# Performance work log

Measured on AMD Instinct MI355X. Metric: run time of the kernel, lower is better.

Reference implementation:

```python
import jax, jax.numpy as jnp
import numpy as np

B, S, D_MODEL, D_FF, NUM_EXPERTS, TOP_K = 2, 2048, 1024, 4096, 8, 2


def setup_inputs() -> dict:
    key = jax.random.key(0)
    ks = jax.random.split(key, 5)
    scale = 0.02
    return {
        "x": jax.random.normal(ks[0], (B, S, D_MODEL), jnp.float32),
        # gate: Linear(d_model, num_experts, bias=False); stored as [d_model, E]
        "Wg": jax.random.normal(ks[1], (D_MODEL, NUM_EXPERTS), jnp.float32) * scale,
        # stacked expert FFN params
        "W1": jax.random.normal(ks[2], (NUM_EXPERTS, D_MODEL, D_FF), jnp.float32) * scale,
        "b1": jnp.zeros((NUM_EXPERTS, D_FF), jnp.float32),
        "W2": jax.random.normal(ks[3], (NUM_EXPERTS, D_FF, D_MODEL), jnp.float32) * scale,
        "b2": jnp.zeros((NUM_EXPERTS, D_MODEL), jnp.float32),
    }


def _moe_forward(x, Wg, W1, b1, W2, b2):
    b, s, d = x.shape
    xt = x.reshape(-1, d)                       # [T, d]
    T = xt.shape[0]
    # --- TopKRouter ---
    probs = jax.nn.softmax(xt @ Wg, axis=-1)    # [T, E]
    w, idx = jax.lax.top_k(probs, TOP_K)        # [T, K]
    w = w / jnp.sum(w, axis=-1, keepdims=True)  # renormalize top-k weights
    # scatter routing weights into dense per-expert combine weights [T, E]
    gate = jnp.zeros((T, Wg.shape[1]), xt.dtype)
    gate = gate.at[jnp.arange(T)[:, None], idx].add(w)
    # --- per-expert FFN, weighted combine (scan over experts, E is small) ---
    def body(out, params):
        W1e, b1e, W2e, b2e, ge = params
        h = jax.nn.relu(xt @ W1e + b1e)         # [T, d_ff]
        out = out + (h @ W2e + b2e) * ge[:, None]
        return out, None
    out0 = jnp.zeros_like(xt)
    out, _ = jax.lax.scan(body, out0, (W1, b1, W2, b2, gate.T))
    return out.reshape(b, s, d)


def reference(x, Wg, W1, b1, W2, b2):
    # eval mode: dropout = identity, load-balance loss = None -> return output only
    return _moe_forward(x, Wg, W1, b1, W2, b2)
```

## Files before the change

### kernel.cpp

```cpp
#include <hip/hip_runtime.h>
#include <hip/hip_bf16.h>
#include <cstdint>
#include <cstddef>

#define T_TOK 4096
#define DM 1024
#define DFF 4096
#define NE 8
#define BT 128
#define BK 64
#define PADCAP (T_TOK * 2 + NE * BT)
#define MTILES (PADCAP / BT)

typedef __attribute__((ext_vector_type(8))) short short8;
typedef __attribute__((ext_vector_type(4))) float f32x4;

__device__ __forceinline__ unsigned short f2bf(float f) {
  unsigned int u = __float_as_uint(f);
  return (unsigned short)((u + 0x7fff + ((u >> 16) & 1)) >> 16);
}
__device__ __forceinline__ float bf2f(unsigned short u) {
  return __uint_as_float((unsigned int)u << 16);
}

__device__ __forceinline__ void load_lds16(const void* g, void* l) {
  __builtin_amdgcn_global_load_lds(
      (const __attribute__((address_space(1))) int*)g,
      (__attribute__((address_space(3))) int*)l, 16, 0, 0);
}

#define WAIT_VM8() __builtin_amdgcn_s_waitcnt(0x0F78)
#define WAIT_VM0() __builtin_amdgcn_s_waitcnt(0x0F70)
#define BARRIER()                          \
  do {                                     \
    __asm__ volatile("" ::: "memory");     \
    __builtin_amdgcn_s_barrier();          \
    __asm__ volatile("" ::: "memory");     \
  } while (0)

__global__ __launch_bounds__(256) void gate_kernel(
    const float* __restrict__ x, const float* __restrict__ Wg,
    int* __restrict__ counts, int* __restrict__ topk_idx,
    float* __restrict__ topk_w, unsigned short* __restrict__ xb) {
  int gid = blockIdx.x * blockDim.x + threadIdx.x;
  int t = gid >> 6;
  int lane = gid & 63;
  if (t >= T_TOK) return;
  const float* xr = x + (size_t)t * DM;
  unsigned short* xbr = xb + (size_t)t * DM;
  float acc[NE];
#pragma unroll
  for (int e = 0; e < NE; ++e) acc[e] = 0.f;
#pragma unroll
  for (int j = 0; j < DM / 64; ++j) {
    int d = lane + j * 64;
    float xv = xr[d];
    xbr[d] = f2bf(xv);
    const float4* wr = (const float4*)(Wg + (size_t)d * NE);
    float4 w0 = wr[0], w1 = wr[1];
    acc[0] += xv * w0.x; acc[1] += xv * w0.y;
    acc[2] += xv * w0.z; acc[3] += xv * w0.w;
    acc[4] += xv * w1.x; acc[5] += xv * w1.y;
    acc[6] += xv * w1.z; acc[7] += xv * w1.w;
  }
#pragma unroll
  for (int off = 32; off >= 1; off >>= 1) {
#pragma unroll
    for (int e = 0; e < NE; ++e) acc[e] += __shfl_xor(acc[e], off, 64);
  }
  if (lane == 0) {
    int i0 = 0;
#pragma unroll
    for (int e = 1; e < NE; ++e)
      if (acc[e] > acc[i0]) i0 = e;
    int i1 = (i0 == 0) ? 1 : 0;
#pragma unroll
    for (int e = 0; e < NE; ++e)
      if (e != i0 && acc[e] > acc[i1]) i1 = e;
    float e1 = __expf(acc[i1] - acc[i0]);
    float inv = 1.f / (1.f + e1);
    topk_idx[t * 2] = i0;
    topk_idx[t * 2 + 1] = i1;
    topk_w[t * 2] = inv;
    topk_w[t * 2 + 1] = e1 * inv;
    atomicAdd(&counts[i0], 1);
    atomicAdd(&counts[i1], 1);
  }
}

__global__ void init_kernel(int* counts, int* cursors, int* bucket_tok) {
  int i = blockIdx.x * blockDim.x + threadIdx.x;
  if (i < NE) { counts[i] = 0; cursors[i] = 0; }
  if (i < PADCAP) bucket_tok[i] = -1;
}

__global__ void offsets_kernel(const int* __restrict__ counts,
                               int* __restrict__ offsets) {
  if (threadIdx.x == 0) {
    int o = 0;
    offsets[0] = 0;
    for (int e = 0; e < NE; ++e) {
      o += (counts[e] + BT - 1) & ~(BT - 1);
      offsets[e + 1] = o;
    }
  }
}

__global__ void scatter_kernel(const int* __restrict__ topk_idx,
                               const int* __restrict__ offsets,
                               int* __restrict__ cursors,
                               int* __restrict__ bucket_tok,
                               int* __restrict__ slot_of) {
  int t = blockIdx.x * blockDim.x + threadIdx.x;
  if (t >= T_TOK) return;
#pragma unroll
  for (int k = 0; k < 2; ++k) {
    int e = topk_idx[t * 2 + k];
    int pos = atomicAdd(&cursors[e], 1);
    int slot = offsets[e] + pos;
    bucket_tok[slot] = t;
    slot_of[t * 2 + k] = slot;
  }
}

__global__ __launch_bounds__(256) void transpose_cvt_kernel(
    const float* __restrict__ W, unsigned short* __restrict__ Wt,
    int K, int N) {
  __shared__ float Ls[64][68];
  int e = blockIdx.z;
  const float* We = W + (size_t)e * K * N;
  unsigned short* Wte = Wt + (size_t)e * K * N;
  int k0 = blockIdx.x * 64, n0 = blockIdx.y * 64;
  int tid = threadIdx.x;
  int kr = tid >> 4, nf = (tid & 15) * 4;
#pragma unroll
  for (int p = 0; p < 4; ++p) {
    int k = kr + p * 16;
    float4 v = *(const float4*)(We + (size_t)(k0 + k) * N + n0 + nf);
    Ls[k][nf] = v.x; Ls[k][nf + 1] = v.y;
    Ls[k][nf + 2] = v.z; Ls[k][nf + 3] = v.w;
  }
  __syncthreads();
#pragma unroll
  for (int i = 0; i < 2; ++i) {
    int id = tid + i * 256;
    int n = id >> 3, kc = id & 7;
    short8 hv;
#pragma unroll
    for (int j = 0; j < 8; ++j) hv[j] = (short)f2bf(Ls[kc * 8 + j][n]);
    *(short8*)(Wte + (size_t)(n0 + n) * K + k0 + kc * 8) = hv;
  }
}


__global__ __launch_bounds__(256) void gemm1_kernel(
    const unsigned short* __restrict__ xb, const unsigned short* __restrict__ Wt1,
    const float* __restrict__ b1, const int* __restrict__ offsets,
    const int* __restrict__ bucket_tok, unsigned short* __restrict__ h) {
  int r0 = blockIdx.x * BT;
  if (r0 >= offsets[NE]) return;
  int e = 0;
  while (offsets[e + 1] <= r0) ++e;
  int n0 = blockIdx.y * 128;

  __shared__ __align__(16) short As[2 * 128 * 64];
  __shared__ __align__(16) short Bs[2 * 128 * 64];
  __shared__ int toks[BT];

  int tid = threadIdx.x;
  if (tid < BT) toks[tid] = bucket_tok[r0 + tid];
  __syncthreads();

  int lane = tid & 63, w = tid >> 6;
  int rsub = lane >> 3, kc = lane & 7;
  int jsw = (kc ^ rsub) * 8;
  const unsigned short* ga[4];
  const unsigned short* gb[4];
#pragma unroll
  for (int i = 0; i < 4; ++i) {
    int m = w * 32 + i * 8 + rsub;
    int tk = toks[m]; if (tk < 0) tk = 0;
    ga[i] = xb + (size_t)tk * DM + jsw;
    gb[i] = Wt1 + ((size_t)e * DFF + n0 + m) * DM + jsw;
  }
  int ldsW = w * 2048 + lane * 8;

  int wm = w & 1, wn = w >> 1;
  int g = lane >> 4, l15 = lane & 15;
  int x7 = l15 & 7;
  int csel0 = (g ^ x7) * 8;
  int csel1 = ((4 + g) ^ x7) * 8;

  f32x4 acc[4][4];
#pragma unroll
  for (int i = 0; i < 4; ++i)
#pragma unroll
    for (int jj = 0; jj < 4; ++jj) acc[i][jj] = (f32x4){0.f, 0.f, 0.f, 0.f};

#pragma unroll
  for (int i = 0; i < 4; ++i) {
    load_lds16(ga[i], &As[ldsW + i * 512]);
    load_lds16(gb[i], &Bs[ldsW + i * 512]);
  }

  int buf = 0;
  const int NIT = DM / BK;
  for (int it = 0; it < NIT; ++it) {
    if (it + 1 < NIT) {
      int ko = (it + 1) * BK;
      int dst = (buf ^ 1) * 8192 + ldsW;
#pragma unroll
      for (int i = 0; i < 4; ++i) {
        load_lds16(ga[i] + ko, &As[dst + i * 512]);
        load_lds16(gb[i] + ko, &Bs[dst + i * 512]);
      }
      WAIT_VM8();
    } else {
      WAIT_VM0();
    }
    BARRIER();
    int bb = buf * 8192;
#pragma unroll
    for (int ks = 0; ks < 2; ++ks) {
      int cs = ks ? csel1 : csel0;
      short8 af[4], bfr[4];
#pragma unroll
      for (int mi = 0; mi < 4; ++mi)
        af[mi] = *(const short8*)&As[bb + (wm * 64 + mi * 16 + l15) * 64 + cs];
#pragma unroll
      for (int nj = 0; nj < 4; ++nj)
        bfr[nj] = *(const short8*)&Bs[bb + (wn * 64 + nj * 16 + l15) * 64 + cs];
#pragma unroll
      for (int mi = 0; mi < 4; ++mi)
#pragma unroll
        for (int nj = 0; nj < 4; ++nj)
          acc[mi][nj] = __builtin_amdgcn_mfma_f32_16x16x32_bf16(
              af[mi], bfr[nj], acc[mi][nj], 0, 0, 0);
    }
    BARRIER();
    buf ^= 1;
  }

  const float* b1e = b1 + (size_t)e * DFF;
#pragma unroll
  for (int nj = 0; nj < 4; ++nj) {
    int n = n0 + wn * 64 + nj * 16 + l15;
    float bv = b1e[n];
#pragma unroll
    for (int mi = 0; mi < 4; ++mi) {
      int mb = r0 + wm * 64 + mi * 16 + g * 4;
#pragma unroll
      for (int r = 0; r < 4; ++r) {
        float v = acc[mi][nj][r] + bv;
        h[(size_t)(mb + r) * DFF + n] = f2bf(fmaxf(v, 0.f));
      }
    }
  }
}

__global__ __launch_bounds__(256) void gemm2_kernel(
    const unsigned short* __restrict__ h, const unsigned short* __restrict__ Wt2,
    const float* __restrict__ b2, const int* __restrict__ offsets,
    unsigned short* __restrict__ S) {
  int r0 = blockIdx.y * BT;
  if (r0 >= offsets[NE]) return;
  int e = 0;
  while (offsets[e + 1] <= r0) ++e;
  int n0 = (blockIdx.x & 7) * 128;
  int z = blockIdx.x >> 3;
  int kbeg = z * (DFF / 2);

  __shared__ __align__(16) short As[2 * 128 * 64];
  __shared__ __align__(16) short Bs[2 * 128 * 64];

  int tid = threadIdx.x;
  int lane = tid & 63, w = tid >> 6;
  int rsub = lane >> 3, kc = lane & 7;
  int jsw = (kc ^ rsub) * 8;
  const unsigned short* ga[4];
  const unsigned short* gb[4];
#pragma unroll
  for (int i = 0; i < 4; ++i) {
    int m = w * 32 + i * 8 + rsub;
    ga[i] = h + ((size_t)(r0 + m)) * DFF + kbeg + jsw;
    gb[i] = Wt2 + ((size_t)e * DM + n0 + m) * DFF + kbeg + jsw;
  }
  int ldsW = w * 2048 + lane * 8;

  int wm = w & 1, wn = w >> 1;
  int g = lane >> 4, l15 = lane & 15;
  int x7 = l15 & 7;
  int csel0 = (g ^ x7) * 8;
  int csel1 = ((4 + g) ^ x7) * 8;

  f32x4 acc[4][4];
#pragma unroll
  for (int i = 0; i < 4; ++i)
#pragma unroll
    for (int jj = 0; jj < 4; ++jj) acc[i][jj] = (f32x4){0.f, 0.f, 0.f, 0.f};

#pragma unroll
  for (int i = 0; i < 4; ++i) {
    load_lds16(ga[i], &As[ldsW + i * 512]);
    load_lds16(gb[i], &Bs[ldsW + i * 512]);
  }

  int buf = 0;
  const int NIT = (DFF / 2) / BK;
  for (int it = 0; it < NIT; ++it) {
    if (it + 1 < NIT) {
      int ko = (it + 1) * BK;
      int dst = (buf ^ 1) * 8192 + ldsW;
#pragma unroll
      for (int i = 0; i < 4; ++i) {
        load_lds16(ga[i] + ko, &As[dst + i * 512]);
        load_lds16(gb[i] + ko, &Bs[dst + i * 512]);
      }
      WAIT_VM8();
    } else {
      WAIT_VM0();
    }
    BARRIER();
    int bb = buf * 8192;
#pragma unroll
    for (int ks = 0; ks < 2; ++ks) {
      int cs = ks ? csel1 : csel0;
      short8 af[4], bfr[4];
#pragma unroll
      for (int mi = 0; mi < 4; ++mi)
        af[mi] = *(const short8*)&As[bb + (wm * 64 + mi * 16 + l15) * 64 + cs];
#pragma unroll
      for (int nj = 0; nj < 4; ++nj)
        bfr[nj] = *(const short8*)&Bs[bb + (wn * 64 + nj * 16 + l15) * 64 + cs];
#pragma unroll
      for (int mi = 0; mi < 4; ++mi)
#pragma unroll
        for (int nj = 0; nj < 4; ++nj)
          acc[mi][nj] = __builtin_amdgcn_mfma_f32_16x16x32_bf16(
              af[mi], bfr[nj], acc[mi][nj], 0, 0, 0);
    }
    BARRIER();
    buf ^= 1;
  }

  const float* b2e = b2 + (size_t)e * DM;
  float bscale = (z == 0) ? 1.f : 0.f;
  unsigned short* Sz = S + (size_t)z * PADCAP * DM;
#pragma unroll
  for (int nj = 0; nj < 4; ++nj) {
    int n = n0 + wn * 64 + nj * 16 + l15;
    float bv = b2e[n] * bscale;
#pragma unroll
    for (int mi = 0; mi < 4; ++mi) {
      int mb = r0 + wm * 64 + mi * 16 + g * 4;
#pragma unroll
      for (int r = 0; r < 4; ++r)
        Sz[(size_t)(mb + r) * DM + n] = f2bf(acc[mi][nj][r] + bv);
    }
  }
}

__global__ __launch_bounds__(256) void combine_kernel(
    const unsigned short* __restrict__ S, const int* __restrict__ slot_of,
    const float* __restrict__ topk_w, float* __restrict__ out) {
  int gid = blockIdx.x * 256 + threadIdx.x;
  int t = gid >> 7;
  int c = (gid & 127) * 8;
  int s0 = slot_of[t * 2], s1 = slot_of[t * 2 + 1];
  float w0 = topk_w[t * 2], w1 = topk_w[t * 2 + 1];
  const short8 a0 = *(const short8*)(S + (size_t)s0 * DM + c);
  const short8 a1 = *(const short8*)(S + ((size_t)PADCAP + s0) * DM + c);
  const short8 b0 = *(const short8*)(S + (size_t)s1 * DM + c);
  const short8 b1 = *(const short8*)(S + ((size_t)PADCAP + s1) * DM + c);
  float o[8];
#pragma unroll
  for (int j = 0; j < 8; ++j) {
    float va = bf2f((unsigned short)a0[j]) + bf2f((unsigned short)a1[j]);
    float vb = bf2f((unsigned short)b0[j]) + bf2f((unsigned short)b1[j]);
    o[j] = w0 * va + w1 * vb;
  }
  float* op = out + (size_t)t * DM + c;
  *(float4*)op = (float4){o[0], o[1], o[2], o[3]};
  *(float4*)(op + 4) = (float4){o[4], o[5], o[6], o[7]};
}

extern "C" void kernel_launch(void* const* d_in, const int* in_sizes, int n_in,
                              void* d_out, int out_size, void* d_ws,
                              size_t ws_size, hipStream_t stream) {
  const float* x = (const float*)d_in[0];
  const float* Wg = (const float*)d_in[1];
  const float* W1 = (const float*)d_in[2];
  const float* b1 = (const float*)d_in[3];
  const float* W2 = (const float*)d_in[4];
  const float* b2 = (const float*)d_in[5];
  float* out = (float*)d_out;

  int* ws_i = (int*)d_ws;
  int* counts = ws_i;
  int* offsets = ws_i + 8;
  int* cursors = ws_i + 20;
  int* bucket_tok = ws_i + 32;
  int* topk_idx = ws_i + 32 + PADCAP;
  float* topk_w = (float*)(ws_i + 32 + PADCAP + 2 * T_TOK);
  int* slot_of = ws_i + 32 + PADCAP + 4 * T_TOK;

  const size_t XB_OFF = 1u << 20;
  const size_t WT_OFF = XB_OFF + (size_t)T_TOK * DM * 2;
  const size_t H_OFF = WT_OFF + (size_t)NE * DM * DFF * 2;
  const size_t S_OFF = H_OFF + (size_t)PADCAP * DFF * 2;
  unsigned short* xb = (unsigned short*)((char*)d_ws + XB_OFF);
  unsigned short* Wt = (unsigned short*)((char*)d_ws + WT_OFF);
  unsigned short* h = (unsigned short*)((char*)d_ws + H_OFF);
  unsigned short* S = (unsigned short*)((char*)d_ws + S_OFF);

  init_kernel<<<(PADCAP + 255) / 256, 256, 0, stream>>>(counts, cursors,
                                                        bucket_tok);
  gate_kernel<<<T_TOK / 4, 256, 0, stream>>>(x, Wg, counts, topk_idx, topk_w,
                                             xb);
  offsets_kernel<<<1, 64, 0, stream>>>(counts, offsets);
  scatter_kernel<<<T_TOK / 256, 256, 0, stream>>>(topk_idx, offsets, cursors,
                                                  bucket_tok, slot_of);
  transpose_cvt_kernel<<<dim3(DM / 64, DFF / 64, NE), 256, 0, stream>>>(
      W1, Wt, DM, DFF);
  gemm1_kernel<<<dim3(MTILES, DFF / 128), 256, 0, stream>>>(
      xb, Wt, b1, offsets, bucket_tok, h);
  transpose_cvt_kernel<<<dim3(DFF / 64, DM / 64, NE), 256, 0, stream>>>(
      W2, Wt, DFF, DM);
  gemm2_kernel<<<dim3(16, MTILES), 256, 0, stream>>>(h, Wt, b2, offsets, S);
  combine_kernel<<<(T_TOK * DM / 8) / 256, 256, 0, stream>>>(S, slot_of,
                                                             topk_w, out);
}
```

Baseline: 710.9 us.

## Halve GEMM K-tile to raise occupancy and stage epilogue stores through LDS

Reduces the K tile of both expert GEMMs from 64 to 32, halving LDS use per block and requesting four blocks per CU via launch bounds, with the swizzle and wait counts adjusted to match. The epilogues now write bf16 results into swizzled LDS tiles and then emit 16-byte coalesced global stores instead of scattered 2-byte stores. The transpose kernel's LDS padding also changes. Smaller K tiles double the barrier count per unit of work, and the higher occupancy target may force register spills.

```diff
diff --git a/kernel.cpp b/kernel.cpp
--- a/kernel.cpp
+++ b/kernel.cpp
@@ -8,7 +8,7 @@
 #define DFF 4096
 #define NE 8
 #define BT 128
-#define BK 64
+#define BK 32
 #define PADCAP (T_TOK * 2 + NE * BT)
 #define MTILES (PADCAP / BT)
 
@@ -29,7 +29,7 @@
       (__attribute__((address_space(3))) int*)l, 16, 0, 0);
 }
 
-#define WAIT_VM8() __builtin_amdgcn_s_waitcnt(0x0F78)
+#define WAIT_VM4() __builtin_amdgcn_s_waitcnt(0x0F74)
 #define WAIT_VM0() __builtin_amdgcn_s_waitcnt(0x0F70)
 #define BARRIER()                          \
   do {                                     \
@@ -126,7 +126,7 @@
 __global__ __launch_bounds__(256) void transpose_cvt_kernel(
     const float* __restrict__ W, unsigned short* __restrict__ Wt,
     int K, int N) {
-  __shared__ float Ls[64][68];
+  __shared__ float Ls[64][67];
   int e = blockIdx.z;
   const float* We = W + (size_t)e * K * N;
   unsigned short* Wte = Wt + (size_t)e * K * N;
@@ -153,7 +153,7 @@
 }
 
 
-__global__ __launch_bounds__(256) void gemm1_kernel(
+__global__ __launch_bounds__(256, 4) void gemm1_kernel(
     const unsigned short* __restrict__ xb, const unsigned short* __restrict__ Wt1,
     const float* __restrict__ b1, const int* __restrict__ offsets,
     const int* __restrict__ bucket_tok, unsigned short* __restrict__ h) {
@@ -163,8 +163,8 @@
   while (offsets[e + 1] <= r0) ++e;
   int n0 = blockIdx.y * 128;
 
-  __shared__ __align__(16) short As[2 * 128 * 64];
-  __shared__ __align__(16) short Bs[2 * 128 * 64];
+  __shared__ __align__(16) short As[2 * 128 * 32];
+  __shared__ __align__(16) short Bs[2 * 128 * 32];
   __shared__ int toks[BT];
 
   int tid = threadIdx.x;
@@ -172,24 +172,22 @@
   __syncthreads();
 
   int lane = tid & 63, w = tid >> 6;
-  int rsub = lane >> 3, kc = lane & 7;
-  int jsw = (kc ^ rsub) * 8;
-  const unsigned short* ga[4];
-  const unsigned short* gb[4];
-#pragma unroll
-  for (int i = 0; i < 4; ++i) {
-    int m = w * 32 + i * 8 + rsub;
+  int rsub = lane >> 2, kc = lane & 3;
+  int jsw = (kc ^ (rsub & 3)) * 8;
+  const unsigned short* ga[2];
+  const unsigned short* gb[2];
+#pragma unroll
+  for (int i = 0; i < 2; ++i) {
+    int m = w * 32 + i * 16 + rsub;
     int tk = toks[m]; if (tk < 0) tk = 0;
     ga[i] = xb + (size_t)tk * DM + jsw;
     gb[i] = Wt1 + ((size_t)e * DFF + n0 + m) * DM + jsw;
   }
-  int ldsW = w * 2048 + lane * 8;
+  int ldsW = w * 1024 + lane * 8;
 
   int wm = w & 1, wn = w >> 1;
   int g = lane >> 4, l15 = lane & 15;
-  int x7 = l15 & 7;
-  int csel0 = (g ^ x7) * 8;
-  int csel1 = ((4 + g) ^ x7) * 8;
+  int cs = (g ^ (l15 & 3)) * 8;
 
   f32x4 acc[4][4];
 #pragma unroll
@@ -198,7 +196,7 @@
     for (int jj = 0; jj < 4; ++jj) acc[i][jj] = (f32x4){0.f, 0.f, 0.f, 0.f};
 
 #pragma unroll
-  for (int i = 0; i < 4; ++i) {
+  for (int i = 0; i < 2; ++i) {
     load_lds16(ga[i], &As[ldsW + i * 512]);
     load_lds16(gb[i], &Bs[ldsW + i * 512]);
   }
@@ -208,57 +206,63 @@
   for (int it = 0; it < NIT; ++it) {
     if (it + 1 < NIT) {
       int ko = (it + 1) * BK;
-      int dst = (buf ^ 1) * 8192 + ldsW;
-#pragma unroll
-      for (int i = 0; i < 4; ++i) {
+      int dst = (buf ^ 1) * 4096 + ldsW;
+#pragma unroll
+      for (int i = 0; i < 2; ++i) {
         load_lds16(ga[i] + ko, &As[dst + i * 512]);
         load_lds16(gb[i] + ko, &Bs[dst + i * 512]);
       }
-      WAIT_VM8();
+      WAIT_VM4();
     } else {
       WAIT_VM0();
     }
     BARRIER();
-    int bb = buf * 8192;
-#pragma unroll
-    for (int ks = 0; ks < 2; ++ks) {
-      int cs = ks ? csel1 : csel0;
-      short8 af[4], bfr[4];
-#pragma unroll
-      for (int mi = 0; mi < 4; ++mi)
-        af[mi] = *(const short8*)&As[bb + (wm * 64 + mi * 16 + l15) * 64 + cs];
+    int bb = buf * 4096;
+    short8 af[4], bfr[4];
+#pragma unroll
+    for (int mi = 0; mi < 4; ++mi)
+      af[mi] = *(const short8*)&As[bb + (wm * 64 + mi * 16 + l15) * 32 + cs];
+#pragma unroll
+    for (int nj = 0; nj < 4; ++nj)
+      bfr[nj] = *(const short8*)&Bs[bb + (wn * 64 + nj * 16 + l15) * 32 + cs];
+#pragma unroll
+    for (int mi = 0; mi < 4; ++mi)
 #pragma unroll
       for (int nj = 0; nj < 4; ++nj)
-        bfr[nj] = *(const short8*)&Bs[bb + (wn * 64 + nj * 16 + l15) * 64 + cs];
-#pragma unroll
-      for (int mi = 0; mi < 4; ++mi)
-#pragma unroll
-        for (int nj = 0; nj < 4; ++nj)
-          acc[mi][nj] = __builtin_amdgcn_mfma_f32_16x16x32_bf16(
-              af[mi], bfr[nj], acc[mi][nj], 0, 0, 0);
-    }
+        acc[mi][nj] = __builtin_amdgcn_mfma_f32_16x16x32_bf16(
+            af[mi], bfr[nj], acc[mi][nj], 0, 0, 0);
     BARRIER();
     buf ^= 1;
   }
 
+  unsigned short* wt =
+      (unsigned short*)(w < 2 ? (void*)As : (void*)Bs) + (w & 1) * 4096;
   const float* b1e = b1 + (size_t)e * DFF;
 #pragma unroll
   for (int nj = 0; nj < 4; ++nj) {
-    int n = n0 + wn * 64 + nj * 16 + l15;
-    float bv = b1e[n];
+    int nl = nj * 16 + l15;
+    float bv = b1e[n0 + wn * 64 + nl];
+    int tchunk = nl >> 3, nin = nl & 7;
 #pragma unroll
     for (int mi = 0; mi < 4; ++mi) {
-      int mb = r0 + wm * 64 + mi * 16 + g * 4;
 #pragma unroll
       for (int r = 0; r < 4; ++r) {
+        int ml = mi * 16 + g * 4 + r;
         float v = acc[mi][nj][r] + bv;
-        h[(size_t)(mb + r) * DFF + n] = f2bf(fmaxf(v, 0.f));
+        wt[ml * 64 + (tchunk ^ (ml & 7)) * 8 + nin] = f2bf(fmaxf(v, 0.f));
       }
     }
   }
-}
-
-__global__ __launch_bounds__(256) void gemm2_kernel(
+  int q = lane >> 3, c = lane & 7;
+#pragma unroll
+  for (int i = 0; i < 8; ++i) {
+    int ml = i * 8 + q;
+    short8 v = *(const short8*)&wt[ml * 64 + (c ^ (ml & 7)) * 8];
+    *(short8*)(h + (size_t)(r0 + wm * 64 + ml) * DFF + n0 + wn * 64 + c * 8) = v;
+  }
+}
+
+__global__ __launch_bounds__(256, 4) void gemm2_kernel(
     const unsigned short* __restrict__ h, const unsigned short* __restrict__ Wt2,
     const float* __restrict__ b2, const int* __restrict__ offsets,
     unsigned short* __restrict__ S) {
@@ -270,28 +274,26 @@
   int z = blockIdx.x >> 3;
   int kbeg = z * (DFF / 2);
 
-  __shared__ __align__(16) short As[2 * 128 * 64];
-  __shared__ __align__(16) short Bs[2 * 128 * 64];
+  __shared__ __align__(16) short As[2 * 128 * 32];
+  __shared__ __align__(16) short Bs[2 * 128 * 32];
 
   int tid = threadIdx.x;
   int lane = tid & 63, w = tid >> 6;
-  int rsub = lane >> 3, kc = lane & 7;
-  int jsw = (kc ^ rsub) * 8;
-  const unsigned short* ga[4];
-  const unsigned short* gb[4];
-#pragma unroll
-  for (int i = 0; i < 4; ++i) {
-    int m = w * 32 + i * 8 + rsub;
+  int rsub = lane >> 2, kc = lane & 3;
+  int jsw = (kc ^ (rsub & 3)) * 8;
+  const unsigned short* ga[2];
+  const unsigned short* gb[2];
+#pragma unroll
+  for (int i = 0; i < 2; ++i) {
+    int m = w * 32 + i * 16 + rsub;
     ga[i] = h + ((size_t)(r0 + m)) * DFF + kbeg + jsw;
     gb[i] = Wt2 + ((size_t)e * DM + n0 + m) * DFF + kbeg + jsw;
   }
-  int ldsW = w * 2048 + lane * 8;
+  int ldsW = w * 1024 + lane * 8;
 
   int wm = w & 1, wn = w >> 1;
   int g = lane >> 4, l15 = lane & 15;
-  int x7 = l15 & 7;
-  int csel0 = (g ^ x7) * 8;
-  int csel1 = ((4 + g) ^ x7) * 8;
+  int cs = (g ^ (l15 & 3)) * 8;
 
   f32x4 acc[4][4];
 #pragma unroll
@@ -300,7 +302,7 @@
     for (int jj = 0; jj < 4; ++jj) acc[i][jj] = (f32x4){0.f, 0.f, 0.f, 0.f};
 
 #pragma unroll
-  for (int i = 0; i < 4; ++i) {
+  for (int i = 0; i < 2; ++i) {
     load_lds16(ga[i], &As[ldsW + i * 512]);
     load_lds16(gb[i], &Bs[ldsW + i * 512]);
   }
@@ -310,53 +312,62 @@
   for (int it = 0; it < NIT; ++it) {
     if (it + 1 < NIT) {
       int ko = (it + 1) * BK;
-      int dst = (buf ^ 1) * 8192 + ldsW;
-#pragma unroll
-      for (int i = 0; i < 4; ++i) {
+      int dst = (buf ^ 1) * 4096 + ldsW;
+#pragma unroll
+      for (int i = 0; i < 2; ++i) {
         load_lds16(ga[i] + ko, &As[dst + i * 512]);
         load_lds16(gb[i] + ko, &Bs[dst + i * 512]);
       }
-      WAIT_VM8();
+      WAIT_VM4();
     } else {
       WAIT_VM0();
     }
     BARRIER();
-    int bb = buf * 8192;
-#pragma unroll
-    for (int ks = 0; ks < 2; ++ks) {
-      int cs = ks ? csel1 : csel0;
-      short8 af[4], bfr[4];
-#pragma unroll
-      for (int mi = 0; mi < 4; ++mi)
-        af[mi] = *(const short8*)&As[bb + (wm * 64 + mi * 16 + l15) * 64 + cs];
+    int bb = buf * 4096;
+    short8 af[4], bfr[4];
+#pragma unroll
+    for (int mi = 0; mi < 4; ++mi)
+      af[mi] = *(const short8*)&As[bb + (wm * 64 + mi * 16 + l15) * 32 + cs];
+#pragma unroll
+    for (int nj = 0; nj < 4; ++nj)
+      bfr[nj] = *(const short8*)&Bs[bb + (wn * 64 + nj * 16 + l15) * 32 + cs];
+#pragma unroll
+    for (int mi = 0; mi < 4; ++mi)
 #pragma unroll
       for (int nj = 0; nj < 4; ++nj)
-        bfr[nj] = *(const short8*)&Bs[bb + (wn * 64 + nj * 16 + l15) * 64 + cs];
-#pragma unroll
-      for (int mi = 0; mi < 4; ++mi)
-#pragma unroll
-        for (int nj = 0; nj < 4; ++nj)
-          acc[mi][nj] = __builtin_amdgcn_mfma_f32_16x16x32_bf16(
-              af[mi], bfr[nj], acc[mi][nj], 0, 0, 0);
-    }
+        acc[mi][nj] = __builtin_amdgcn_mfma_f32_16x16x32_bf16(
+            af[mi], bfr[nj], acc[mi][nj], 0, 0, 0);
     BARRIER();
     buf ^= 1;
   }
 
+  unsigned short* wt =
+      (unsigned short*)(w < 2 ? (void*)As : (void*)Bs) + (w & 1) * 4096;
   const float* b2e = b2 + (size_t)e * DM;
   float bscale = (z == 0) ? 1.f : 0.f;
   unsigned short* Sz = S + (size_t)z * PADCAP * DM;
 #pragma unroll
   for (int nj = 0; nj < 4; ++nj) {
-    int n = n0 + wn * 64 + nj * 16 + l15;
-    float bv = b2e[n] * bscale;
+    int nl = nj * 16 + l15;
+    float bv = b2e[n0 + wn * 64 + nl] * bscale;
+    int tchunk = nl >> 3, nin = nl & 7;
 #pragma unroll
     for (int mi = 0; mi < 4; ++mi) {
-      int mb = r0 + wm * 64 + mi * 16 + g * 4;
-#pragma unroll
-      for (int r = 0; r < 4; ++r)
-        Sz[(size_t)(mb + r) * DM + n] = f2bf(acc[mi][nj][r] + bv);
+#pragma unroll
+      for (int r = 0; r < 4; ++r) {
+        int ml = mi * 16 + g * 4 + r;
+        wt[ml * 64 + (tchunk ^ (ml & 7)) * 8 + nin] =
+            f2bf(acc[mi][nj][r] + bv);
+      }
     }
+  }
+  int q = lane >> 3, c = lane & 7;
+#pragma unroll
+  for (int i = 0; i < 8; ++i) {
+    int ml = i * 8 + q;
+    short8 v = *(const short8*)&wt[ml * 64 + (c ^ (ml & 7)) * 8];
+    *(short8*)(Sz + (size_t)(r0 + wm * 64 + ml) * DM + n0 + wn * 64 + c * 8) =
+        v;
   }
 }
 
```

After: 720.0 us. About the same (+1.3%).
